# Optimization experiments

Measured on AMD Instinct MI355X. Metric: run time of the kernel, lower is better.

The kernel has to match this reference:

```python
import jax, jax.numpy as jnp
import numpy as np

# module config (matches init_kwargs)
H, W, C = 32, 32, 3
KH, KW, KC = 4, 4, 1
N_CLASS = 10
NBIN = 200
SHIFT = (0, 0)
NH, NW, NC = H // KH, W // KW, C // KC
NKERNEL = NH * NW * NC          # 192
NDIM_SUB = KH * KW * KC         # 16
NCOMP = NDIM_SUB                # n_component defaults to ndim_sub
NDIM = H * W * C                # 3072
NTRANS = NKERNEL * NCOMP        # 3072
N = 2048


def setup_inputs() -> dict:
    key = jax.random.key(0)
    k1, k2, k3, k4, k5, k6 = jax.random.split(key, 6)
    data = jax.random.normal(k1, (N, NDIM), dtype=jnp.float32)
    label = jax.random.randint(k2, (N,), 0, N_CLASS)
    # per-patch orthonormal projections: QR with sign fix, as in __init__
    wi = jax.random.normal(k3, (NKERNEL, NDIM_SUB, NCOMP), dtype=jnp.float32)
    Q, R = jnp.linalg.qr(wi)
    sign = jnp.sign(jnp.diagonal(R, axis1=-2, axis2=-1))
    wT_blocks = Q * sign[:, None, :]
    # monotone rational-quadratic spline knots per class / transformed dim
    dx = jax.random.uniform(k4, (N_CLASS, NTRANS, NBIN - 1), minval=0.5, maxval=1.5)
    dy = jax.random.uniform(k5, (N_CLASS, NTRANS, NBIN - 1), minval=0.5, maxval=1.5)
    z = jnp.zeros((N_CLASS, NTRANS, 1), jnp.float32)
    knots_x = -4.0 + 8.0 * jnp.concatenate([z, jnp.cumsum(dx, -1)], -1) / jnp.sum(dx, -1, keepdims=True)
    knots_y = -4.0 + 8.0 * jnp.concatenate([z, jnp.cumsum(dy, -1)], -1) / jnp.sum(dy, -1, keepdims=True)
    knots_d = jax.random.uniform(k6, (N_CLASS, NTRANS, NBIN), minval=0.5, maxval=1.5)
    return {"data": data, "label": label, "wT_blocks": wT_blocks,
            "knots_x": knots_x.astype(jnp.float32), "knots_y": knots_y.astype(jnp.float32),
            "knots_d": knots_d}


def construct_wT(wT_blocks):
    """Assemble block-structured (NDIM, NTRANS) projection from per-patch blocks."""
    dim = jnp.arange(NDIM).reshape(H, W, C)
    dim = jnp.roll(dim, (-SHIFT[0], -SHIFT[1]), axis=(0, 1))  # Shift() == negative roll
    # rows[b] = flat pixel indices of patch b; block order index = h*NW*NC + w*NC + c
    rows = dim.reshape(NH, KH, NW, KW, C).transpose(0, 2, 4, 1, 3).reshape(NKERNEL, NDIM_SUB)
    cols = jnp.arange(NKERNEL)[:, None] * NCOMP + jnp.arange(NCOMP)[None, :]
    wT = jnp.zeros((NDIM, NTRANS), wT_blocks.dtype)
    return wT.at[rows[:, :, None], cols[:, None, :]].set(wT_blocks)


def rq_spline(x, xx, yy, dd):
    """Monotone rational-quadratic spline with linear extrapolation.
    x: (N, T); xx/yy/dd: (T, K) knot positions / values / derivatives.
    Returns (y, log|dy/dx|), each (N, T)."""
    xT = x.T  # (T, N)
    lo, hi = xx[:, :1], xx[:, -1:]
    below, above = xT < lo, xT > hi
    xc = jnp.clip(xT, lo, hi)  # keep interior branch NaN-free
    k = jax.vmap(lambda kn, v: jnp.searchsorted(kn, v, side='right'))(xx, xc) - 1
    k = jnp.clip(k, 0, NBIN - 2)
    take = lambda a, i: jnp.take_along_axis(a, i, axis=1)
    xk, xk1 = take(xx, k), take(xx, k + 1)
    yk, yk1 = take(yy, k), take(yy, k + 1)
    dk, dk1 = take(dd, k), take(dd, k + 1)
    wdt = xk1 - xk
    s = (yk1 - yk) / wdt
    xi = (xc - xk) / wdt
    om = 1.0 - xi
    denom = s + (dk1 + dk - 2.0 * s) * xi * om
    ys = yk + (yk1 - yk) * (s * xi * xi + dk * xi * om) / denom
    lj_s = 2.0 * jnp.log(s) + jnp.log(dk1 * xi * xi + 2.0 * s * xi * om + dk * om * om) - 2.0 * jnp.log(denom)
    d0, dK = dd[:, :1], dd[:, -1:]
    y = jnp.where(below, yy[:, :1] + (xT - lo) * d0,
                  jnp.where(above, yy[:, -1:] + (xT - hi) * dK, ys))
    lj = jnp.where(below, jnp.log(d0), jnp.where(above, jnp.log(dK), lj_s))
    return y.T, lj.T


def reference(data, label, wT_blocks, knots_x, knots_y, knots_d):
    wT = construct_wT(wT_blocks)                 # (NDIM, NTRANS)
    data0 = data @ wT                            # (N, NTRANS)
    remaining = data - data0 @ wT.T              # orthogonal complement (zero here since full-rank)

    def body(carry, params):
        c, data1, logj = carry
        xx, yy, dd = params
        y, lj = rq_spline(data0, xx, yy, dd)
        m = label == c
        data1 = jnp.where(m[:, None], y, data1)
        logj = jnp.where(m, jnp.sum(lj, axis=1), logj)
        return (c + 1, data1, logj), None

    init = (jnp.int32(0), jnp.zeros_like(data0), jnp.zeros((data.shape[0],), data.dtype))
    (_, data1, logj), _ = jax.lax.scan(body, init, (knots_x, knots_y, knots_d))
    out = remaining + data1 @ wT.T
    return out, logj
```

## Files before the change

kernel.cpp:

```cpp
#include <hip/hip_runtime.h>

constexpr int NSAMP  = 2048;
constexpr int NDIM   = 3072;
constexpr int NTRANS = 3072;
constexpr int NBIN   = 200;
constexpr int NCLASS = 10;
constexpr int NPATCH = 192;
constexpr int BLK    = 256;
constexpr int PER_T  = NDIM / BLK;
constexpr int DSTR   = 20;
constexpr int SA     = 4;
constexpr int SC     = 4;
constexpr int NL     = 128;
constexpr int LUTS   = 136;

__device__ __forceinline__ float4* xb_line(float* xb, int p, int sl) {
    return (float4*)(xb + ((size_t)p * NSAMP + (sl ^ (p & 63))) * 16);
}
__device__ __forceinline__ const float4* xb_line_c(const float* xb, int p, int sl) {
    return (const float4*)(xb + ((size_t)p * NSAMP + (sl ^ (p & 63))) * 16);
}

__global__ __launch_bounds__(1024)
void p0_prep(const int* __restrict__ label,
             int* __restrict__ slot,
             int* __restrict__ cls_off,
             float* __restrict__ logj_slot)
{
    __shared__ int s_lab[NSAMP];
    __shared__ int s_cnt[32][NCLASS];
    __shared__ int s_pre[32][NCLASS];
    __shared__ int s_tot[NCLASS];
    __shared__ int s_off[NCLASS + 1];
    const int tid  = threadIdx.x;
    const int lane = tid & 63;
    const int wv   = tid >> 6;

    for (int i = tid; i < NSAMP; i += 1024) {
        s_lab[i] = label[i];
        logj_slot[i] = 0.f;
    }
    __syncthreads();

    const unsigned long long ltmask = ((unsigned long long)1 << lane) - 1;
    int myrank[2], myc[2];
    #pragma unroll
    for (int pass = 0; pass < 2; ++pass) {
        const int n = pass * 1024 + tid;
        const int c = s_lab[n];
        myc[pass] = c;
        int r = 0;
        #pragma unroll
        for (int cls = 0; cls < NCLASS; ++cls) {
            const unsigned long long b = __ballot(c == cls);
            if (lane == 0) s_cnt[pass * 16 + wv][cls] = __popcll(b);
            if (cls == c)  r = __popcll(b & ltmask);
        }
        myrank[pass] = r;
    }
    __syncthreads();

    if (tid < 32 * NCLASS) {
        const int seg = tid & 31;
        const int cls = tid >> 5;
        int acc = 0;
        for (int s = 0; s < seg; ++s) acc += s_cnt[s][cls];
        s_pre[seg][cls] = acc;
        if (seg == 31) s_tot[cls] = acc + s_cnt[31][cls];
    }
    __syncthreads();
    if (tid == 0) {
        int a = 0;
        for (int c = 0; c < NCLASS; ++c) { s_off[c] = a; a += s_tot[c]; }
        s_off[NCLASS] = a;
    }
    __syncthreads();

    #pragma unroll
    for (int pass = 0; pass < 2; ++pass) {
        const int n   = pass * 1024 + tid;
        const int seg = pass * 16 + wv;
        const int c   = myc[pass];
        slot[n] = s_off[c] + s_pre[seg][c] + myrank[pass];
    }
    if (tid <= NCLASS) cls_off[tid] = s_off[tid];
}

__global__ __launch_bounds__(BLK, 4)
void pA_project(const float* __restrict__ data,
                const float* __restrict__ B,
                const int*   __restrict__ slot,
                float* __restrict__ xb)
{
    __shared__ float s_data[SA][NDIM];
    const int b   = blockIdx.x;
    const int tid = threadIdx.x;
    const int n0  = b * SA;

    #pragma unroll
    for (int s = 0; s < SA; ++s) {
        const float4* dr = (const float4*)(data + (size_t)(n0 + s) * NDIM);
        float4* sd = (float4*)s_data[s];
        #pragma unroll
        for (int j = 0; j < 3; ++j)
            sd[tid + BLK * j] = dr[tid + BLK * j];
    }
    int sls[SA];
    #pragma unroll
    for (int s = 0; s < SA; ++s) sls[s] = slot[n0 + s];
    __syncthreads();

    #pragma unroll 1
    for (int jj = 0; jj < 3; ++jj) {
        const int tau = tid + BLK * jj;
        const int p   = tau >> 2;
        const int q4  = tau & 3;
        const int nh  = p / 24;
        const int rem = p - nh * 24;
        const int nw  = rem / 3;
        const int ch  = rem - nw * 3;
        const int rowbase = nh * 384 + nw * 12 + ch;

        float4 Bp[16];
        const float4* Bg = (const float4*)(B + p * 256 + q4 * 4);
        #pragma unroll
        for (int i = 0; i < 16; ++i) Bp[i] = Bg[i * 4];

        #pragma unroll
        for (int s = 0; s < SA; ++s) {
            float dv[16];
            #pragma unroll
            for (int i = 0; i < 16; ++i)
                dv[i] = s_data[s][rowbase + (i >> 2) * 96 + (i & 3) * 3];

            float acc[4] = {0.f, 0.f, 0.f, 0.f};
            #pragma unroll
            for (int i = 0; i < 16; ++i) {
                acc[0] += Bp[i].x * dv[i];
                acc[1] += Bp[i].y * dv[i];
                acc[2] += Bp[i].z * dv[i];
                acc[3] += Bp[i].w * dv[i];
            }
            *(xb_line(xb, p, sls[s]) + q4) =
                make_float4(acc[0], acc[1], acc[2], acc[3]);
        }
    }
}

__global__ __launch_bounds__(BLK, 8)
void pB_spline(const float* __restrict__ kx,
               const float* __restrict__ ky,
               const float* __restrict__ kd,
               const int*   __restrict__ cls_off,
               float* __restrict__ xb,
               float* __restrict__ logj_slot)
{
    __shared__ float s_kx[16 * NBIN];
    __shared__ unsigned char s_lut[16 * LUTS];

    const int p   = blockIdx.x;
    const int c   = blockIdx.y;
    const int tid = threadIdx.x;
    const int t0  = p * 16;

    const size_t kofs = ((size_t)c * NTRANS + t0) * NBIN;
    const float4* gx = (const float4*)(kx + kofs);
    float4* lx = (float4*)s_kx;
    #pragma unroll 1
    for (int i = tid; i < 16 * NBIN / 4; i += BLK) lx[i] = gx[i];
    __syncthreads();

    {
        const int r  = tid >> 4;
        const int ch = tid & 15;
        const float* xx = s_kx + r * NBIN;
        const int j0 = ch * 8;
        const float xu0 = -4.0f + (float)j0 * (8.0f / NL);
        int klo = 0, khi = NBIN;
        #pragma unroll
        for (int it = 0; it < 8; ++it) {
            const int mid = (klo + khi) >> 1;
            const bool le = (xx[mid] <= xu0);
            klo = le ? mid : klo;
            khi = le ? khi : mid;
        }
        int k = klo;
        const int nj = (ch == 15) ? 9 : 8;
        unsigned char* lrow = s_lut + r * LUTS + j0;
        #pragma unroll 1
        for (int jj = 0; jj < nj; ++jj) {
            const float xuj = -4.0f + (float)(j0 + jj) * (8.0f / NL);
            while (k < NBIN - 1 && xx[k + 1] <= xuj) ++k;
            lrow[jj] = (unsigned char)k;
        }
    }
    __syncthreads();

    const int qq  = tid & 3;
    const int sid = tid >> 2;
    const float* sxx = s_kx + qq * 4 * NBIN;
    const float* kyp = ky + kofs + (size_t)(qq * 4) * NBIN;
    const float* kdp = kd + kofs + (size_t)(qq * 4) * NBIN;

    const int beg = cls_off[c];
    const int end = cls_off[c + 1];
    const int nit = (end - beg + 63) >> 6;

    int sl = beg + sid;
    float4 v = make_float4(0.f, 0.f, 0.f, 0.f);
    float4* lcur = nullptr;
    if (sl < end) { lcur = xb_line(xb, p, sl) + qq; v = *lcur; }

    #pragma unroll 1
    for (int it = 0; it < nit; ++it) {
        const int sln = sl + 64;
        float4 vn = make_float4(0.f, 0.f, 0.f, 0.f);
        float4* lnx = nullptr;
        if (it + 1 < nit && sln < end) { lnx = xb_line(xb, p, sln) + qq; vn = *lnx; }

        if (lcur) {
            float xs[4] = {v.x, v.y, v.z, v.w};
            float lj_sum = 0.f;
            #pragma unroll
            for (int j = 0; j < 4; ++j) {
                const float* xx  = sxx + j * NBIN;
                const float* yyg = kyp + j * NBIN;
                const float* ddg = kdp + j * NBIN;
                const unsigned char* lrow = s_lut + (qq * 4 + j) * LUTS;
                const float x  = xs[j];
                const float lo = xx[0];
                const float hi = xx[NBIN - 1];

                float y, lj;
                if (x < lo) {
                    const float d0 = ddg[0];
                    y  = yyg[0] + (x - lo) * d0;
                    lj = __logf(d0);
                } else if (x > hi) {
                    const float dK = ddg[NBIN - 1];
                    y  = yyg[NBIN - 1] + (x - hi) * dK;
                    lj = __logf(dK);
                } else {
                    int u = (int)((x + 4.0f) * (NL / 8.0f));
                    u = u < 0 ? 0 : (u > NL - 1 ? NL - 1 : u);
                    int klo = (int)lrow[u] - 1;
                    klo = klo < 0 ? 0 : klo;
                    int khi = (int)lrow[u + 1] + 2;
                    khi = khi > NBIN ? NBIN : khi;
                    #pragma unroll
                    for (int itb = 0; itb < 3; ++itb) {
                        const int mid = (klo + khi) >> 1;
                        const bool le = (xx[mid] <= x);
                        klo = le ? mid : klo;
                        khi = le ? khi : mid;
                    }
                    int k = klo;
                    if (k > NBIN - 2) k = NBIN - 2;

                    const float xk = xx[k], xk1 = xx[k + 1];
                    const float yk = yyg[k], yk1 = yyg[k + 1];
                    const float dk = ddg[k], dk1 = ddg[k + 1];

                    const float wdt     = xk1 - xk;
                    const float inv_wdt = __fdividef(1.f, wdt);
                    const float dy      = yk1 - yk;
                    const float s       = dy * inv_wdt;
                    const float xi      = (x - xk) * inv_wdt;
                    const float om      = 1.f - xi;
                    const float denom   = s + (dk1 + dk - 2.f * s) * xi * om;
                    const float r       = __fdividef(1.f, denom);
                    const float num     = dy * (s * xi * xi + dk * xi * om);
                    y = yk + num * r;
                    const float Nq = dk1 * xi * xi + 2.f * s * xi * om + dk * om * om;
                    const float t2 = s * r;
                    lj = __logf(t2 * t2 * Nq);
                }
                xs[j] = y - x;
                lj_sum += lj;
            }

            *lcur = make_float4(xs[0], xs[1], xs[2], xs[3]);

            lj_sum += __shfl_xor(lj_sum, 1);
            lj_sum += __shfl_xor(lj_sum, 2);
            if (qq == 0) atomicAdd(&logj_slot[sl], lj_sum);
        }

        sl = sln; lcur = lnx; v = vn;
    }
}

__global__ __launch_bounds__(BLK, 2)
void pC_recon(const float* __restrict__ data,
              const float* __restrict__ B,
              const int*   __restrict__ slot,
              const float* __restrict__ xb,
              const float* __restrict__ logj_slot,
              float* __restrict__ out,
              float* __restrict__ logj)
{
    __shared__ float s_diff[SC][NPATCH * DSTR];
    const int b   = blockIdx.x;
    const int tid = threadIdx.x;
    const int n0  = b * SC;

    #pragma unroll
    for (int s = 0; s < SC; ++s) {
        const int sl = slot[n0 + s];
        #pragma unroll
        for (int jj = 0; jj < 3; ++jj) {
            const int i  = tid + BLK * jj;
            const int pp = i >> 2;
            const int q  = i & 3;
            const float4 v = *(xb_line_c(xb, pp, sl) + q);
            *(float4*)&s_diff[s][pp * DSTR + q * 4] = v;
        }
    }
    if (tid < SC) logj[n0 + tid] = logj_slot[slot[n0 + tid]];
    __syncthreads();

    #pragma unroll 1
    for (int j = 0; j < PER_T; ++j) {
        const int d  = tid + BLK * j;
        const int ch = d % 3;
        const int hw = d / 3;
        const int w  = hw & 31;
        const int h  = hw >> 5;
        const int p  = ((h >> 2) * 8 + (w >> 2)) * 3 + ch;
        const int i  = (h & 3) * 4 + (w & 3);

        const float4* Bp4 = (const float4*)(B + p * 256 + i * 16);
        const float4 b0 = Bp4[0], b1 = Bp4[1], b2 = Bp4[2], b3 = Bp4[3];

        #pragma unroll
        for (int s = 0; s < SC; ++s) {
            const float4* dp4 = (const float4*)&s_diff[s][p * DSTR];
            const float4 d0 = dp4[0], d1 = dp4[1], d2 = dp4[2], d3 = dp4[3];
            float acc = data[(size_t)(n0 + s) * NDIM + d];
            acc += b0.x * d0.x + b0.y * d0.y + b0.z * d0.z + b0.w * d0.w;
            acc += b1.x * d1.x + b1.y * d1.y + b1.z * d1.z + b1.w * d1.w;
            acc += b2.x * d2.x + b2.y * d2.y + b2.z * d2.z + b2.w * d2.w;
            acc += b3.x * d3.x + b3.y * d3.y + b3.z * d3.z + b3.w * d3.w;
            out[(size_t)(n0 + s) * NDIM + d] = acc;
        }
    }
}

extern "C" void kernel_launch(void* const* d_in, const int* in_sizes, int n_in,
                              void* d_out, int out_size, void* d_ws, size_t ws_size,
                              hipStream_t stream) {
    const float* data  = (const float*)d_in[0];
    const int*   label = (const int*)  d_in[1];
    const float* B     = (const float*)d_in[2];
    const float* kx    = (const float*)d_in[3];
    const float* ky    = (const float*)d_in[4];
    const float* kd    = (const float*)d_in[5];

    float* out  = (float*)d_out;
    float* logj = (float*)d_out + (size_t)NSAMP * NDIM;

    char* ws = (char*)d_ws;
    size_t off = 0;
    float* xb        = (float*)(ws + off); off += (size_t)NPATCH * NSAMP * 16 * 4;
    float* logj_slot = (float*)(ws + off); off += NSAMP * 4;
    int*   slot      = (int*)  (ws + off); off += NSAMP * 4;
    int*   cls_off   = (int*)  (ws + off); off += 64;

    p0_prep   <<<1, 1024, 0, stream>>>(label, slot, cls_off, logj_slot);
    pA_project<<<NSAMP / SA, BLK, 0, stream>>>(data, B, slot, xb);
    dim3 gridB(NPATCH, NCLASS);
    pB_spline <<<gridB, BLK, 0, stream>>>(kx, ky, kd, cls_off, xb, logj_slot);
    pC_recon  <<<NSAMP / SC, BLK, 0, stream>>>(data, B, slot, xb, logj_slot, out, logj);
}
```

Before: 199.8 us.

## Use sample-major intermediate layout and finer bin LUT with linear scan

Changes the intermediate projection buffer from a patch-major swizzled layout to a plain sample-major layout, so each sample's transformed vector is contiguous. The spline lookup table grows from 128 to 1024 entries per dimension, which lets the binary search be replaced by a fixed 6-knot window and a branch-free count. The aim is fewer dependent shared-memory lookups per spline evaluation and more contiguous writes and reads in the reconstruction stage. The cost is more shared memory and a longer LUT build, with occupancy hint lowered to 5. Correctness relies on the true bin falling inside the 6-knot window, which holds only if knot spacing is not too tight relative to the LUT resolution.

```diff
diff --git a/kernel.cpp b/kernel.cpp
--- a/kernel.cpp
+++ b/kernel.cpp
@@ -11,14 +11,14 @@
 constexpr int DSTR   = 20;
 constexpr int SA     = 4;
 constexpr int SC     = 4;
-constexpr int NL     = 128;
-constexpr int LUTS   = 136;
-
-__device__ __forceinline__ float4* xb_line(float* xb, int p, int sl) {
-    return (float4*)(xb + ((size_t)p * NSAMP + (sl ^ (p & 63))) * 16);
-}
-__device__ __forceinline__ const float4* xb_line_c(const float* xb, int p, int sl) {
-    return (const float4*)(xb + ((size_t)p * NSAMP + (sl ^ (p & 63))) * 16);
+constexpr int NL     = 1024;
+constexpr int LUTS   = 1032;
+
+__device__ __forceinline__ float4* xb_ptr(float* xb, int sl, int t4) {
+    return (float4*)(xb + (size_t)sl * NTRANS) + t4;
+}
+__device__ __forceinline__ const float4* xb_ptr_c(const float* xb, int sl, int t4) {
+    return (const float4*)(xb + (size_t)sl * NTRANS) + t4;
 }
 
 __global__ __launch_bounds__(1024)
@@ -141,13 +141,13 @@
                 acc[2] += Bp[i].z * dv[i];
                 acc[3] += Bp[i].w * dv[i];
             }
-            *(xb_line(xb, p, sls[s]) + q4) =
+            *xb_ptr(xb, sls[s], tau) =
                 make_float4(acc[0], acc[1], acc[2], acc[3]);
         }
     }
 }
 
-__global__ __launch_bounds__(BLK, 8)
+__global__ __launch_bounds__(BLK, 5)
 void pB_spline(const float* __restrict__ kx,
                const float* __restrict__ ky,
                const float* __restrict__ kd,
@@ -174,7 +174,7 @@
         const int r  = tid >> 4;
         const int ch = tid & 15;
         const float* xx = s_kx + r * NBIN;
-        const int j0 = ch * 8;
+        const int j0 = ch * 64;
         const float xu0 = -4.0f + (float)j0 * (8.0f / NL);
         int klo = 0, khi = NBIN;
         #pragma unroll
@@ -185,7 +185,7 @@
             khi = le ? khi : mid;
         }
         int k = klo;
-        const int nj = (ch == 15) ? 9 : 8;
+        const int nj = (ch == 15) ? 65 : 64;
         unsigned char* lrow = s_lut + r * LUTS + j0;
         #pragma unroll 1
         for (int jj = 0; jj < nj; ++jj) {
@@ -209,14 +209,14 @@
     int sl = beg + sid;
     float4 v = make_float4(0.f, 0.f, 0.f, 0.f);
     float4* lcur = nullptr;
-    if (sl < end) { lcur = xb_line(xb, p, sl) + qq; v = *lcur; }
+    if (sl < end) { lcur = xb_ptr(xb, sl, p * 4 + qq); v = *lcur; }
 
     #pragma unroll 1
     for (int it = 0; it < nit; ++it) {
         const int sln = sl + 64;
         float4 vn = make_float4(0.f, 0.f, 0.f, 0.f);
         float4* lnx = nullptr;
-        if (it + 1 < nit && sln < end) { lnx = xb_line(xb, p, sln) + qq; vn = *lnx; }
+        if (it + 1 < nit && sln < end) { lnx = xb_ptr(xb, sln, p * 4 + qq); vn = *lnx; }
 
         if (lcur) {
             float xs[4] = {v.x, v.y, v.z, v.w};
@@ -244,20 +244,21 @@
                     int u = (int)((x + 4.0f) * (NL / 8.0f));
                     u = u < 0 ? 0 : (u > NL - 1 ? NL - 1 : u);
                     int klo = (int)lrow[u] - 1;
-                    klo = klo < 0 ? 0 : klo;
-                    int khi = (int)lrow[u + 1] + 2;
-                    khi = khi > NBIN ? NBIN : khi;
-                    #pragma unroll
-                    for (int itb = 0; itb < 3; ++itb) {
-                        const int mid = (klo + khi) >> 1;
-                        const bool le = (xx[mid] <= x);
-                        klo = le ? mid : klo;
-                        khi = le ? khi : mid;
-                    }
-                    int k = klo;
-                    if (k > NBIN - 2) k = NBIN - 2;
-
-                    const float xk = xx[k], xk1 = xx[k + 1];
+                    klo = klo < 0 ? 0 : (klo > NBIN - 6 ? NBIN - 6 : klo);
+                    const float v0 = xx[klo];
+                    const float v1 = xx[klo + 1];
+                    const float v2 = xx[klo + 2];
+                    const float v3 = xx[klo + 3];
+                    const float v4 = xx[klo + 4];
+                    const float v5 = xx[klo + 5];
+                    const int cnt = (int)(v1 <= x) + (int)(v2 <= x)
+                                  + (int)(v3 <= x) + (int)(v4 <= x);
+                    const int k = klo + cnt;
+                    const float xk  = cnt == 0 ? v0 : cnt == 1 ? v1 :
+                                      cnt == 2 ? v2 : cnt == 3 ? v3 : v4;
+                    const float xk1 = cnt == 0 ? v1 : cnt == 1 ? v2 :
+                                      cnt == 2 ? v3 : cnt == 3 ? v4 : v5;
+
                     const float yk = yyg[k], yk1 = yyg[k + 1];
                     const float dk = ddg[k], dk1 = ddg[k + 1];
 
@@ -312,7 +313,7 @@
             const int i  = tid + BLK * jj;
             const int pp = i >> 2;
             const int q  = i & 3;
-            const float4 v = *(xb_line_c(xb, pp, sl) + q);
+            const float4 v = *xb_ptr_c(xb, sl, i);
             *(float4*)&s_diff[s][pp * DSTR + q * 4] = v;
         }
     }
@@ -361,7 +362,7 @@
 
     char* ws = (char*)d_ws;
     size_t off = 0;
-    float* xb        = (float*)(ws + off); off += (size_t)NPATCH * NSAMP * 16 * 4;
+    float* xb        = (float*)(ws + off); off += (size_t)NSAMP * NTRANS * 4;
     float* logj_slot = (float*)(ws + off); off += NSAMP * 4;
     int*   slot      = (int*)  (ws + off); off += NSAMP * 4;
     int*   cls_off   = (int*)  (ws + off); off += 64;
```

Measured after the change: 236.4 us. 18.3% more time.

## Split reconstruction kernel into quarter-dimension blocks for more parallelism

Applied to the files above, without the earlier changes.

The reconstruction kernel now launches a 2D grid where each block handles 4 samples and one quarter of the output dimensions (48 patches, 768 dims). This shrinks shared memory per block and raises the launch bounds' target occupancy, giving four times as many blocks to hide memory latency. Each block loads only the patch coefficients it needs. In exchange, the per-block slot lookups and setup are repeated across quarters.

```diff
diff --git a/kernel.cpp b/kernel.cpp
--- a/kernel.cpp
+++ b/kernel.cpp
@@ -7,10 +7,11 @@
 constexpr int NCLASS = 10;
 constexpr int NPATCH = 192;
 constexpr int BLK    = 256;
-constexpr int PER_T  = NDIM / BLK;
 constexpr int DSTR   = 20;
 constexpr int SA     = 4;
 constexpr int SC     = 4;
+constexpr int QP     = 48;
+constexpr int QD     = 768;
 constexpr int NL     = 128;
 constexpr int LUTS   = 136;
 
@@ -290,7 +291,7 @@
     }
 }
 
-__global__ __launch_bounds__(BLK, 2)
+__global__ __launch_bounds__(BLK, 8)
 void pC_recon(const float* __restrict__ data,
               const float* __restrict__ B,
               const int*   __restrict__ slot,
@@ -299,34 +300,39 @@
               float* __restrict__ out,
               float* __restrict__ logj)
 {
-    __shared__ float s_diff[SC][NPATCH * DSTR];
-    const int b   = blockIdx.x;
+    __shared__ float s_diff[SC][QP * DSTR];
+    const int g   = blockIdx.x;
+    const int qtr = blockIdx.y;
     const int tid = threadIdx.x;
-    const int n0  = b * SC;
-
-    #pragma unroll
-    for (int s = 0; s < SC; ++s) {
-        const int sl = slot[n0 + s];
-        #pragma unroll
-        for (int jj = 0; jj < 3; ++jj) {
-            const int i  = tid + BLK * jj;
-            const int pp = i >> 2;
-            const int q  = i & 3;
-            const float4 v = *(xb_line_c(xb, pp, sl) + q);
-            *(float4*)&s_diff[s][pp * DSTR + q * 4] = v;
-        }
-    }
-    if (tid < SC) logj[n0 + tid] = logj_slot[slot[n0 + tid]];
+    const int n0  = g * SC;
+    const int pq  = qtr * QP;
+
+    int sls[SC];
+    #pragma unroll
+    for (int s = 0; s < SC; ++s) sls[s] = slot[n0 + s];
+
+    #pragma unroll
+    for (int jj = 0; jj < 3; ++jj) {
+        const int e  = tid + BLK * jj;
+        const int s  = e / (QP * 4);
+        const int r  = e - s * (QP * 4);
+        const int pl = r >> 2;
+        const int q  = r & 3;
+        const float4 v = *(xb_line_c(xb, pq + pl, sls[s]) + q);
+        *(float4*)&s_diff[s][pl * DSTR + q * 4] = v;
+    }
+    if (qtr == 0 && tid < SC) logj[n0 + tid] = logj_slot[sls[tid]];
     __syncthreads();
 
     #pragma unroll 1
-    for (int j = 0; j < PER_T; ++j) {
-        const int d  = tid + BLK * j;
+    for (int j = 0; j < QD / BLK; ++j) {
+        const int d  = qtr * QD + tid + BLK * j;
         const int ch = d % 3;
         const int hw = d / 3;
         const int w  = hw & 31;
         const int h  = hw >> 5;
         const int p  = ((h >> 2) * 8 + (w >> 2)) * 3 + ch;
+        const int pl = p - pq;
         const int i  = (h & 3) * 4 + (w & 3);
 
         const float4* Bp4 = (const float4*)(B + p * 256 + i * 16);
@@ -334,7 +340,7 @@
 
         #pragma unroll
         for (int s = 0; s < SC; ++s) {
-            const float4* dp4 = (const float4*)&s_diff[s][p * DSTR];
+            const float4* dp4 = (const float4*)&s_diff[s][pl * DSTR];
             const float4 d0 = dp4[0], d1 = dp4[1], d2 = dp4[2], d3 = dp4[3];
             float acc = data[(size_t)(n0 + s) * NDIM + d];
             acc += b0.x * d0.x + b0.y * d0.y + b0.z * d0.z + b0.w * d0.w;
@@ -370,5 +376,6 @@
     pA_project<<<NSAMP / SA, BLK, 0, stream>>>(data, B, slot, xb);
     dim3 gridB(NPATCH, NCLASS);
     pB_spline <<<gridB, BLK, 0, stream>>>(kx, ky, kd, cls_off, xb, logj_slot);
-    pC_recon  <<<NSAMP / SC, BLK, 0, stream>>>(data, B, slot, xb, logj_slot, out, logj);
-}
+    dim3 gridC(NSAMP / SC, NDIM / QD);
+    pC_recon  <<<gridC, BLK, 0, stream>>>(data, B, slot, xb, logj_slot, out, logj);
+}
```

After: 198.3 us. No clear change (-0.8%).
